# Kernel optimization log

Measured on AMD Instinct MI355X. Metric: run time of the kernel, lower is better.

## Reference

```python
import jax, jax.numpy as jnp
import numpy as np

N_NODES = 50000
N_EDGES = 600000
FEAT = 128
N_LAYERS = 4


def setup_inputs() -> dict:
    key = jax.random.key(0)
    ks = jax.random.split(key, 7)
    feats = jax.random.normal(ks[0], (N_NODES, FEAT), dtype=jnp.float32)
    src = jax.random.randint(ks[1], (N_EDGES,), 0, N_NODES)
    dst = jax.random.randint(ks[2], (N_EDGES,), 0, N_NODES)
    s = 1.0 / np.sqrt(FEAT)  # torch Linear default init range
    theta_w = jax.random.uniform(ks[3], (N_LAYERS, FEAT, FEAT), jnp.float32, -s, s)
    theta_b = jax.random.uniform(ks[4], (N_LAYERS, FEAT), jnp.float32, -s, s)
    phi_w = jax.random.uniform(ks[5], (N_LAYERS, FEAT, FEAT), jnp.float32, -s, s)
    phi_b = jax.random.uniform(ks[6], (N_LAYERS, FEAT), jnp.float32, -s, s)
    return {"feats": feats, "src": src, "dst": dst,
            "theta_w": theta_w, "theta_b": theta_b,
            "phi_w": phi_w, "phi_b": phi_b}


def _edgeconv(x, src, dst, tw, tb, pw, pb):
    # EdgeConv (Wang et al. 2018): out_i = max_{(j->i) in E} theta(x_j - x_i) + phi(x_i)
    phi = x @ pw.T + pb                       # [N, F] node-level linear (avoid per-edge recompute)
    diff = x[src] - x[dst]                    # [E, F] gather
    msg = diff @ tw.T + tb + phi[dst]         # [E, F]
    agg = jax.ops.segment_max(msg, dst, num_segments=x.shape[0])  # [N, F]
    # nodes with no incoming edges get -inf from segment_max; zero them (DGL convention)
    return jnp.where(jnp.isneginf(agg), jnp.zeros_like(agg), agg)


def reference(feats, src, dst, theta_w, theta_b, phi_w, phi_b):
    x = feats
    for l in range(N_LAYERS):
        x = _edgeconv(x, src, dst, theta_w[l], theta_b[l], phi_w[l], phi_b[l])
        x = jax.nn.relu(x)
    return x
```

## Files before the change

kernel.cpp:

```cpp
#include <hip/hip_runtime.h>

#define FEAT 128

typedef __attribute__((ext_vector_type(8))) _Float16 f16x8;
typedef __attribute__((ext_vector_type(2))) _Float16 f16x2;
typedef __attribute__((ext_vector_type(4))) float f32x4;

static __device__ __forceinline__ int wave_incl_scan(int v, int lane) {
#pragma unroll
    for (int off = 1; off < 64; off <<= 1) {
        int u = __shfl_up(v, off, 64);
        if (lane >= off) v += u;
    }
    return v;
}


__global__ void hist_kernel(const int* __restrict__ dst, int* __restrict__ deg, int E) {
    int e = blockIdx.x * blockDim.x + threadIdx.x;
    if (e < E) atomicAdd(&deg[dst[e]], 1);
}

__global__ __launch_bounds__(1024) void scan1_kernel(const int* __restrict__ deg,
                                                     int* __restrict__ row_ptr,
                                                     int* __restrict__ bsum, int N) {
    int i = blockIdx.x * 1024 + threadIdx.x;
    int lane = threadIdx.x & 63;
    int w = threadIdx.x >> 6;
    int v = (i < N) ? deg[i] : 0;
    int inc = wave_incl_scan(v, lane);
    __shared__ int wsum[16];
    if (lane == 63) wsum[w] = inc;
    __syncthreads();
    if (w == 0) {
        int s = (lane < 16) ? wsum[lane] : 0;
        int si = wave_incl_scan(s, lane);
        if (lane < 16) wsum[lane] = si - s;
    }
    __syncthreads();
    int exc = inc - v + wsum[w];
    if (i < N) row_ptr[i] = exc;
    if (threadIdx.x == 1023) bsum[blockIdx.x] = exc + v;
}

__global__ __launch_bounds__(1024) void scan2_kernel(const int* __restrict__ bsum,
                                                     int* __restrict__ boff,
                                                     int* __restrict__ row_ptr,
                                                     int nb, int N, int E) {
    int tid = threadIdx.x;
    int lane = tid & 63;
    int w = tid >> 6;
    int v = (tid < nb) ? bsum[tid] : 0;
    int inc = wave_incl_scan(v, lane);
    __shared__ int wsum[16];
    if (lane == 63) wsum[w] = inc;
    __syncthreads();
    if (w == 0) {
        int s = (lane < 16) ? wsum[lane] : 0;
        int si = wave_incl_scan(s, lane);
        if (lane < 16) wsum[lane] = si - s;
    }
    __syncthreads();
    if (tid < nb) boff[tid] = inc - v + wsum[w];
    if (tid == 0) row_ptr[N] = E;
}

__global__ void scan3_kernel(int* __restrict__ row_ptr, const int* __restrict__ boff, int N) {
    int i = blockIdx.x * blockDim.x + threadIdx.x;
    if (i < N) row_ptr[i] += boff[i >> 10];
}

__global__ void scatter_kernel(const int* __restrict__ src, const int* __restrict__ dst,
                               const int* __restrict__ row_ptr, int* __restrict__ fill,
                               int* __restrict__ esrc, int E) {
    int e = blockIdx.x * blockDim.x + threadIdx.x;
    if (e < E) {
        int d = dst[e];
        int pos = row_ptr[d] + atomicAdd(&fill[d], 1);
        esrc[pos] = src[e];
    }
}


__global__ void wcvt_kernel(const float* __restrict__ tw, const float* __restrict__ pw,
                            const float* __restrict__ tb, const float* __restrict__ pb,
                            _Float16* __restrict__ wt, _Float16* __restrict__ wp,
                            float* __restrict__ bsum, int n, int nbias) {
    int i = blockIdx.x * blockDim.x + threadIdx.x;
    if (i < n) { wt[i] = (_Float16)tw[i]; wp[i] = (_Float16)pw[i]; }
    if (i < nbias) bsum[i] = tb[i] + pb[i];
}

__global__ void xcvt_kernel(const float* __restrict__ x, _Float16* __restrict__ x16, int n4) {
    int i = blockIdx.x * blockDim.x + threadIdx.x;
    if (i < n4) {
        float4 v = ((const float4*)x)[i];
        f16x2 a, b;
        a[0] = (_Float16)v.x; a[1] = (_Float16)v.y;
        b[0] = (_Float16)v.z; b[1] = (_Float16)v.w;
        ((f16x2*)x16)[i * 2] = a;
        ((f16x2*)x16)[i * 2 + 1] = b;
    }
}


__global__ __launch_bounds__(256) void mfma_gemm_kernel(
        const _Float16* __restrict__ x16,
        const _Float16* __restrict__ wt, const _Float16* __restrict__ wp,
        const float* __restrict__ bias,
        _Float16* __restrict__ t16, _Float16* __restrict__ q16, int M) {
    int lane = threadIdx.x & 63;
    int l16 = lane & 15;
    int quad = lane >> 4;
    int cn0 = (threadIdx.x >> 6) * 32;

    f16x8 bt[2][4], bp[2][4];
    float biasv[2];
#pragma unroll
    for (int ct = 0; ct < 2; ++ct) {
        int col = cn0 + ct * 16 + l16;
        biasv[ct] = bias[col];
#pragma unroll
        for (int kk = 0; kk < 4; ++kk) {
            int k = kk * 32 + quad * 8;
            bt[ct][kk] = *(const f16x8*)(wt + (size_t)col * FEAT + k);
            bp[ct][kk] = *(const f16x8*)(wp + (size_t)col * FEAT + k);
        }
    }

    int rbase0 = blockIdx.x * 128;
#pragma unroll 1
    for (int rs = 0; rs < 8; ++rs) {
        int rbase = rbase0 + rs * 16;
        int row = rbase + l16;
        int rowc = (row < M) ? row : (M - 1);
        f16x8 a[4];
#pragma unroll
        for (int kk = 0; kk < 4; ++kk)
            a[kk] = *(const f16x8*)(x16 + (size_t)rowc * FEAT + kk * 32 + quad * 8);

        f32x4 accT[2] = {{0.f, 0.f, 0.f, 0.f}, {0.f, 0.f, 0.f, 0.f}};
        f32x4 accP[2] = {{0.f, 0.f, 0.f, 0.f}, {0.f, 0.f, 0.f, 0.f}};
#pragma unroll
        for (int kk = 0; kk < 4; ++kk) {
#pragma unroll
            for (int ct = 0; ct < 2; ++ct) {
                accT[ct] = __builtin_amdgcn_mfma_f32_16x16x32_f16(a[kk], bt[ct][kk], accT[ct], 0, 0, 0);
                accP[ct] = __builtin_amdgcn_mfma_f32_16x16x32_f16(a[kk], bp[ct][kk], accP[ct], 0, 0, 0);
            }
        }
#pragma unroll
        for (int ct = 0; ct < 2; ++ct) {
            int col = cn0 + ct * 16 + l16;
#pragma unroll
            for (int r = 0; r < 4; ++r) {
                int ro = rbase + quad * 4 + r;
                if (ro < M) {
                    t16[(size_t)ro * FEAT + col] = (_Float16)accT[ct][r];
                    q16[(size_t)ro * FEAT + col] =
                        (_Float16)(accP[ct][r] - accT[ct][r] + biasv[ct]);
                }
            }
        }
    }
}


static __device__ __forceinline__ f16x8 vmax8(f16x8 a, f16x8 b) {
#pragma unroll
    for (int i = 0; i < 8; ++i) a[i] = (a[i] > b[i]) ? a[i] : b[i];
    return a;
}

static __device__ __forceinline__ f16x8 shflxor8(f16x8 v, int mask) {
    union { f16x8 h; int i[4]; } u;
    u.h = v;
#pragma unroll
    for (int k = 0; k < 4; ++k) u.i[k] = __shfl_xor(u.i[k], mask, 64);
    return u.h;
}

__global__ __launch_bounds__(256) void agg_kernel(
        const _Float16* __restrict__ t16, const _Float16* __restrict__ q16,
        const int* __restrict__ row_ptr, const int* __restrict__ esrc,
        float* __restrict__ outf, _Float16* __restrict__ ox, int N) {
    int wv = threadIdx.x >> 6;
    int lane = threadIdx.x & 63;
    int node = blockIdx.x * 4 + wv;
    if (node >= N) return;

    int g = lane >> 4;
    int c = lane & 15;

    int beg = row_ptr[node];
    int end = row_ptr[node + 1];

    if (beg >= end) {
        if (outf && g == 0) {
            float4 z = make_float4(0.f, 0.f, 0.f, 0.f);
            ((float4*)(outf + (size_t)node * FEAT + c * 8))[0] = z;
            ((float4*)(outf + (size_t)node * FEAT + c * 8))[1] = z;
        }
        if (ox && g == 0) {
            f16x8 z = {};
            *(f16x8*)(ox + (size_t)node * FEAT + c * 8) = z;
        }
        return;
    }

    const _Float16 NEGINF = (_Float16)(-65504.0f);
    f16x8 m;
#pragma unroll
    for (int i = 0; i < 8; ++i) m[i] = NEGINF;

    for (int base = beg; base < end; base += 64) {
        int n = end - base;
        if (n > 64) n = 64;
        int nm1 = n - 1;
        int li = (lane < n) ? lane : nm1;
        int myidx = esrc[base + li];
        int j = 0;
        for (; j + 8 <= n; j += 8) {
            int i0 = __shfl(myidx, j + g);
            int i1 = __shfl(myidx, j + 4 + g);
            f16x8 v0 = *(const f16x8*)(t16 + (size_t)i0 * FEAT + c * 8);
            f16x8 v1 = *(const f16x8*)(t16 + (size_t)i1 * FEAT + c * 8);
            m = vmax8(m, vmax8(v0, v1));
        }
        for (; j < n; j += 4) {
            int sl = j + g;
            if (sl > nm1) sl = nm1;
            int idx = __shfl(myidx, sl);
            f16x8 v = *(const f16x8*)(t16 + (size_t)idx * FEAT + c * 8);
            m = vmax8(m, v);
        }
    }

    m = vmax8(m, shflxor8(m, 16));
    m = vmax8(m, shflxor8(m, 32));

    if (g == 0) {
        f16x8 qi = *(const f16x8*)(q16 + (size_t)node * FEAT + c * 8);
        float o[8];
#pragma unroll
        for (int i = 0; i < 8; ++i)
            o[i] = fmaxf((float)m[i] + (float)qi[i], 0.f);

        if (outf) {
            float4 o0 = make_float4(o[0], o[1], o[2], o[3]);
            float4 o1 = make_float4(o[4], o[5], o[6], o[7]);
            ((float4*)(outf + (size_t)node * FEAT + c * 8))[0] = o0;
            ((float4*)(outf + (size_t)node * FEAT + c * 8))[1] = o1;
        }
        if (ox) {
            f16x8 oh;
#pragma unroll
            for (int i = 0; i < 8; ++i) oh[i] = (_Float16)o[i];
            *(f16x8*)(ox + (size_t)node * FEAT + c * 8) = oh;
        }
    }
}


extern "C" void kernel_launch(void* const* d_in, const int* in_sizes, int n_in,
                              void* d_out, int out_size, void* d_ws, size_t ws_size,
                              hipStream_t stream) {
    const float* feats   = (const float*)d_in[0];
    const int*   src     = (const int*)d_in[1];
    const int*   dst     = (const int*)d_in[2];
    const float* theta_w = (const float*)d_in[3];
    const float* theta_b = (const float*)d_in[4];
    const float* phi_w   = (const float*)d_in[5];
    const float* phi_b   = (const float*)d_in[6];

    const int N = in_sizes[0] / FEAT;
    const int E = in_sizes[1];
    const int L = in_sizes[3] / (FEAT * FEAT);

    char* ws = (char*)d_ws;
    size_t off = 0;
    auto alloc = [&](size_t bytes) -> void* {
        void* ptr = ws + off;
        off = (off + bytes + 255) & ~(size_t)255;
        return ptr;
    };
    _Float16* t16 = (_Float16*)alloc((size_t)N * FEAT * 2);
    _Float16* q16 = (_Float16*)alloc((size_t)N * FEAT * 2);
    _Float16* x16 = (_Float16*)alloc((size_t)N * FEAT * 2);
    _Float16* wt16 = (_Float16*)alloc((size_t)L * FEAT * FEAT * 2);
    _Float16* wp16 = (_Float16*)alloc((size_t)L * FEAT * FEAT * 2);
    float* bsum_b = (float*)alloc((size_t)L * FEAT * sizeof(float));
    int* deg     = (int*)alloc((size_t)N * sizeof(int));
    int* fill    = (int*)alloc((size_t)N * sizeof(int));
    int* row_ptr = (int*)alloc((size_t)(N + 1) * sizeof(int));
    int* esrc    = (int*)alloc((size_t)E * sizeof(int));
    int* bsum    = (int*)alloc(2048 * sizeof(int));
    int* boff    = (int*)alloc(2048 * sizeof(int));
    (void)ws_size;

    hipMemsetAsync(deg, 0, (size_t)N * sizeof(int), stream);
    hipMemsetAsync(fill, 0, (size_t)N * sizeof(int), stream);

    int eb = (E + 255) / 256;
    int nb = (N + 1023) >> 10;
    hist_kernel<<<eb, 256, 0, stream>>>(dst, deg, E);
    scan1_kernel<<<nb, 1024, 0, stream>>>(deg, row_ptr, bsum, N);
    scan2_kernel<<<1, 1024, 0, stream>>>(bsum, boff, row_ptr, nb, N, E);
    scan3_kernel<<<(N + 255) / 256, 256, 0, stream>>>(row_ptr, boff, N);
    scatter_kernel<<<eb, 256, 0, stream>>>(src, dst, row_ptr, fill, esrc, E);

    int wn = L * FEAT * FEAT;
    wcvt_kernel<<<(wn + 255) / 256, 256, 0, stream>>>(
        theta_w, phi_w, theta_b, phi_b, wt16, wp16, bsum_b, wn, L * FEAT);
    int xn4 = N * FEAT / 4;
    xcvt_kernel<<<(xn4 + 255) / 256, 256, 0, stream>>>(feats, x16, xn4);

    int gb = (N + 127) / 128;
    for (int l = 0; l < L; ++l) {
        mfma_gemm_kernel<<<gb, 256, 0, stream>>>(
            x16,
            wt16 + (size_t)l * FEAT * FEAT,
            wp16 + (size_t)l * FEAT * FEAT,
            bsum_b + (size_t)l * FEAT,
            t16, q16, N);

        bool last = (l == L - 1);
        agg_kernel<<<(N + 3) / 4, 256, 0, stream>>>(
            t16, q16,
            row_ptr, esrc,
            last ? (float*)d_out : nullptr,
            last ? nullptr : x16,
            N);
    }
}
```

Measured before the change: 341.5 us.

## Fuse edge scatter into first GEMM launch and unroll aggregation gathers fourfold

The CSR edge scatter now shares a single launch with the layer-0 GEMM through block-index partitioning, so one kernel launch goes away and the two independent workloads can run concurrently. The aggregation loop now issues up to four predicated gathers per 16-edge step into separate max accumulators, which keeps more memory loads in flight. The cost is extra registers in the aggregation kernel and a heterogeneous fused kernel whose launch bounds follow the GEMM path.

```diff
diff --git a/kernel.cpp b/kernel.cpp
--- a/kernel.cpp
+++ b/kernel.cpp
@@ -70,17 +70,6 @@
     if (i < N) row_ptr[i] += boff[i >> 10];
 }
 
-__global__ void scatter_kernel(const int* __restrict__ src, const int* __restrict__ dst,
-                               const int* __restrict__ row_ptr, int* __restrict__ fill,
-                               int* __restrict__ esrc, int E) {
-    int e = blockIdx.x * blockDim.x + threadIdx.x;
-    if (e < E) {
-        int d = dst[e];
-        int pos = row_ptr[d] + atomicAdd(&fill[d], 1);
-        esrc[pos] = src[e];
-    }
-}
-
 
 __global__ void wcvt_kernel(const float* __restrict__ tw, const float* __restrict__ pw,
                             const float* __restrict__ tb, const float* __restrict__ pb,
@@ -104,7 +93,8 @@
 }
 
 
-__global__ __launch_bounds__(256) void mfma_gemm_kernel(
+static __device__ __forceinline__ void gemm_body(
+        int bx,
         const _Float16* __restrict__ x16,
         const _Float16* __restrict__ wt, const _Float16* __restrict__ wp,
         const float* __restrict__ bias,
@@ -128,7 +118,7 @@
         }
     }
 
-    int rbase0 = blockIdx.x * 128;
+    int rbase0 = bx * 128;
 #pragma unroll 1
     for (int rs = 0; rs < 8; ++rs) {
         int rbase = rbase0 + rs * 16;
@@ -161,6 +151,34 @@
                         (_Float16)(accP[ct][r] - accT[ct][r] + biasv[ct]);
                 }
             }
+        }
+    }
+}
+
+__global__ __launch_bounds__(256) void mfma_gemm_kernel(
+        const _Float16* __restrict__ x16,
+        const _Float16* __restrict__ wt, const _Float16* __restrict__ wp,
+        const float* __restrict__ bias,
+        _Float16* __restrict__ t16, _Float16* __restrict__ q16, int M) {
+    gemm_body(blockIdx.x, x16, wt, wp, bias, t16, q16, M);
+}
+
+__global__ __launch_bounds__(256) void fused0_kernel(
+        const _Float16* __restrict__ x16,
+        const _Float16* __restrict__ wt, const _Float16* __restrict__ wp,
+        const float* __restrict__ bias,
+        _Float16* __restrict__ t16, _Float16* __restrict__ q16, int M, int gb,
+        const int* __restrict__ src, const int* __restrict__ dst,
+        const int* __restrict__ row_ptr, int* __restrict__ fill,
+        int* __restrict__ esrc, int E) {
+    if ((int)blockIdx.x < gb) {
+        gemm_body(blockIdx.x, x16, wt, wp, bias, t16, q16, M);
+    } else {
+        int e = (blockIdx.x - gb) * 256 + threadIdx.x;
+        if (e < E) {
+            int d = dst[e];
+            int pos = row_ptr[d] + atomicAdd(&fill[d], 1);
+            esrc[pos] = src[e];
         }
     }
 }
@@ -209,9 +227,9 @@
     }
 
     const _Float16 NEGINF = (_Float16)(-65504.0f);
-    f16x8 m;
-#pragma unroll
-    for (int i = 0; i < 8; ++i) m[i] = NEGINF;
+    f16x8 m0, m1, m2, m3;
+#pragma unroll
+    for (int i = 0; i < 8; ++i) { m0[i] = NEGINF; m1[i] = NEGINF; m2[i] = NEGINF; m3[i] = NEGINF; }
 
     for (int base = beg; base < end; base += 64) {
         int n = end - base;
@@ -219,22 +237,31 @@
         int nm1 = n - 1;
         int li = (lane < n) ? lane : nm1;
         int myidx = esrc[base + li];
-        int j = 0;
-        for (; j + 8 <= n; j += 8) {
-            int i0 = __shfl(myidx, j + g);
-            int i1 = __shfl(myidx, j + 4 + g);
-            f16x8 v0 = *(const f16x8*)(t16 + (size_t)i0 * FEAT + c * 8);
-            f16x8 v1 = *(const f16x8*)(t16 + (size_t)i1 * FEAT + c * 8);
-            m = vmax8(m, vmax8(v0, v1));
-        }
-        for (; j < n; j += 4) {
-            int sl = j + g;
-            if (sl > nm1) sl = nm1;
-            int idx = __shfl(myidx, sl);
-            f16x8 v = *(const f16x8*)(t16 + (size_t)idx * FEAT + c * 8);
-            m = vmax8(m, v);
-        }
-    }
+        for (int j = 0; j < n; j += 16) {
+            bool b1 = (j + 4) < n, b2 = (j + 8) < n, b3 = (j + 12) < n;
+            int s0 = j + g;       if (s0 > nm1) s0 = nm1;
+            f16x8 v0 = *(const f16x8*)(t16 + (size_t)__shfl(myidx, s0) * FEAT + c * 8);
+            f16x8 v1, v2, v3;
+            if (b1) {
+                int s1 = j + 4 + g;  if (s1 > nm1) s1 = nm1;
+                v1 = *(const f16x8*)(t16 + (size_t)__shfl(myidx, s1) * FEAT + c * 8);
+            }
+            if (b2) {
+                int s2 = j + 8 + g;  if (s2 > nm1) s2 = nm1;
+                v2 = *(const f16x8*)(t16 + (size_t)__shfl(myidx, s2) * FEAT + c * 8);
+            }
+            if (b3) {
+                int s3 = j + 12 + g; if (s3 > nm1) s3 = nm1;
+                v3 = *(const f16x8*)(t16 + (size_t)__shfl(myidx, s3) * FEAT + c * 8);
+            }
+            m0 = vmax8(m0, v0);
+            if (b1) m1 = vmax8(m1, v1);
+            if (b2) m2 = vmax8(m2, v2);
+            if (b3) m3 = vmax8(m3, v3);
+        }
+    }
+
+    f16x8 m = vmax8(vmax8(m0, m1), vmax8(m2, m3));
 
     m = vmax8(m, shflxor8(m, 16));
     m = vmax8(m, shflxor8(m, 32));
@@ -307,7 +334,6 @@
     scan1_kernel<<<nb, 1024, 0, stream>>>(deg, row_ptr, bsum, N);
     scan2_kernel<<<1, 1024, 0, stream>>>(bsum, boff, row_ptr, nb, N, E);
     scan3_kernel<<<(N + 255) / 256, 256, 0, stream>>>(row_ptr, boff, N);
-    scatter_kernel<<<eb, 256, 0, stream>>>(src, dst, row_ptr, fill, esrc, E);
 
     int wn = L * FEAT * FEAT;
     wcvt_kernel<<<(wn + 255) / 256, 256, 0, stream>>>(
@@ -317,12 +343,18 @@
 
     int gb = (N + 127) / 128;
     for (int l = 0; l < L; ++l) {
-        mfma_gemm_kernel<<<gb, 256, 0, stream>>>(
-            x16,
-            wt16 + (size_t)l * FEAT * FEAT,
-            wp16 + (size_t)l * FEAT * FEAT,
-            bsum_b + (size_t)l * FEAT,
-            t16, q16, N);
+        if (l == 0) {
+            fused0_kernel<<<gb + eb, 256, 0, stream>>>(
+                x16, wt16, wp16, bsum_b, t16, q16, N, gb,
+                src, dst, row_ptr, fill, esrc, E);
+        } else {
+            mfma_gemm_kernel<<<gb, 256, 0, stream>>>(
+                x16,
+                wt16 + (size_t)l * FEAT * FEAT,
+                wp16 + (size_t)l * FEAT * FEAT,
+                bsum_b + (size_t)l * FEAT,
+                t16, q16, N);
+        }
 
         bool last = (l == L - 1);
         agg_kernel<<<(N + 3) / 4, 256, 0, stream>>>(
```

New measurement: 338.9 us. About the same (-0.8%).
